# Optimization experiments

Hardware: AMD Instinct MI355X
Metric: run time of the kernel (lower is better)

## Reference

```python
import jax, jax.numpy as jnp
import numpy as np

H, C = 6, 32  # heads, per-head channels (concat=False -> mean over heads)
NEG_SLOPE = 0.2


def gat_layer(x, edge_index, W, a_src, a_dst, b):
    # PyG GATConv (shared lin, add_self_loops=True, concat=False, bias)
    N = x.shape[0]
    xh = (x @ W).reshape(N, H, C)                      # [N,H,C]
    alpha_src = (xh * a_src).sum(-1)                   # [N,H]
    alpha_dst = (xh * a_dst).sum(-1)                   # [N,H]
    loops = jnp.arange(N, dtype=edge_index.dtype)
    src = jnp.concatenate([edge_index[0], loops])
    dst = jnp.concatenate([edge_index[1], loops])
    e = jax.nn.leaky_relu(alpha_src[src] + alpha_dst[dst], NEG_SLOPE)  # [E,H]
    # segment softmax over incoming edges of each destination node
    m = jax.ops.segment_max(e, dst, num_segments=N)
    e = jnp.exp(e - m[dst])
    denom = jax.ops.segment_sum(e, dst, num_segments=N)
    alpha = e / (denom[dst] + 1e-16)                   # [E,H]
    out = jax.ops.segment_sum(alpha[:, :, None] * xh[src], dst, num_segments=N)  # [N,H,C]
    return out.mean(axis=1) + b                        # [N,C]


def setup_inputs() -> dict:
    key = jax.random.key(0)
    ks = jax.random.split(key, 20)
    B, E = 50000, 800000
    NU, NI, D = 100000, 50000, 32
    s = 0.1
    inp = {}
    inp['user'] = jax.random.randint(ks[0], (B,), 0, NU)
    inp['item'] = jax.random.randint(ks[1], (B,), 0, NI)
    inp['graph'] = jax.random.randint(ks[2], (2, E), 0, B)
    inp['u_table'] = jax.random.normal(ks[3], (NU, D), jnp.float32) * s
    inp['i_table'] = jax.random.normal(ks[4], (NI, D), jnp.float32) * s
    # GAT layer 1: in=32 -> heads*32
    inp['W1'] = jax.random.normal(ks[5], (D, H * C), jnp.float32) * s
    inp['a_src1'] = jax.random.normal(ks[6], (H, C), jnp.float32) * s
    inp['a_dst1'] = jax.random.normal(ks[7], (H, C), jnp.float32) * s
    inp['b1'] = jnp.zeros((C,), jnp.float32)
    # GAT layer 2: in=32 -> heads*32
    inp['W2'] = jax.random.normal(ks[8], (C, H * C), jnp.float32) * s
    inp['a_src2'] = jax.random.normal(ks[9], (H, C), jnp.float32) * s
    inp['a_dst2'] = jax.random.normal(ks[10], (H, C), jnp.float32) * s
    inp['b2'] = jnp.zeros((C,), jnp.float32)
    # MLP head: (C + D)=64 -> 64 -> 1
    inp['lw1'] = jax.random.normal(ks[11], (C + D, 64), jnp.float32) * s
    inp['lb1'] = jnp.zeros((64,), jnp.float32)
    inp['lw2'] = jax.random.normal(ks[12], (64, 1), jnp.float32) * s
    inp['lb2'] = jnp.zeros((1,), jnp.float32)
    return inp


def reference(user, item, graph, u_table, i_table, W1, a_src1, a_dst1, b1,
              W2, a_src2, a_dst2, b2, lw1, lb1, lw2, lb2):
    u_emb = u_table[user]                              # [B, 32]
    i_emb = i_table[item]                              # [B, 32]
    i_emb = gat_layer(i_emb, graph, W1, a_src1, a_dst1, b1)
    i_emb = gat_layer(i_emb, graph, W2, a_src2, a_dst2, b2)
    out = jnp.concatenate([u_emb, i_emb], axis=1)      # [B, 64]
    out = out @ lw1 + lb1
    out = out @ lw2 + lb2                              # [B, 1]
    return jax.nn.sigmoid(out)
```

## Files before the change

### kernel.cpp

```cpp
#include <hip/hip_runtime.h>
#include <hip/hip_fp16.h>
#include <math.h>

#define NEG_SLOPE 0.2f
#define TILE 16
#define BKB2 8
#define CHUNK 16384

__global__ void k_init(
    const float* __restrict__ W1, const float* __restrict__ as1,
    const float* __restrict__ ad1,
    const float* __restrict__ W2, const float* __restrict__ as2,
    const float* __restrict__ ad2,
    const float* __restrict__ lw1, const float* __restrict__ lb1,
    const float* __restrict__ lw2, const float* __restrict__ lb2,
    float* __restrict__ wsd1, float* __restrict__ wsd2,
    float* __restrict__ weff,
    unsigned int* __restrict__ whalf1, unsigned int* __restrict__ whalf2,
    int* __restrict__ bcnt, int NBK)
{
    int t = threadIdx.x;
    if (t <= NBK) bcnt[t] = 0;
    if (t < 768) {
        int layer = (t >= 384);
        int r = t - layer * 384;
        int k = r / 12, j = r - k * 12;
        const float* W = layer ? W2 : W1;
        const float* a = (j < 6) ? (layer ? as2 : as1) : (layer ? ad2 : ad1);
        int h = (j < 6) ? j : j - 6;
        float acc = 0.f;
        #pragma unroll
        for (int c = 0; c < 32; ++c)
            acc = fmaf(W[k * 192 + h * 32 + c], a[h * 32 + c], acc);
        (layer ? wsd2 : wsd1)[k * 12 + j] = acc;
    } else {
        int i = t - 768;
        float acc = 0.f;
        for (int o = 0; o < 64; ++o) acc += lw1[i * 64 + o] * lw2[o];
        weff[i] = acc;
        if (i == 0) {
            float b = lb2[0];
            for (int o = 0; o < 64; ++o) b += lb1[o] * lw2[o];
            weff[64] = b;
        }
    }
    if (t < 384) {
        int layer = (t >= 192);
        int col = t - layer * 192;
        const float* W = layer ? W2 : W1;
        unsigned int* dst = layer ? whalf2 : whalf1;
        #pragma unroll
        for (int i = 0; i < 16; ++i) {
            __half2 p = __floats2half2_rn(W[(2 * i) * 192 + col],
                                          W[(2 * i + 1) * 192 + col]);
            dst[col * 16 + i] = *(unsigned int*)&p;
        }
    }
}

__global__ __launch_bounds__(256) void k_hist_prep(
    const int* __restrict__ g, int E, int* __restrict__ bcnt,
    int* __restrict__ blockbase, int NBK, int NBLK,
    const float* __restrict__ xf, const int* __restrict__ gidx,
    const float* __restrict__ wsd, __half* __restrict__ xp,
    float* __restrict__ asrc, float* __restrict__ adst, int N)
{
    __shared__ int hist[256];
    __shared__ float xs[TILE * 33];
    __shared__ int   rows[TILE];
    __shared__ float wsd_s[384];
    const int t = threadIdx.x;
    if (blockIdx.x < NBLK) {
        const int blk = blockIdx.x;
        hist[t] = 0;
        __syncthreads();
        const int base = blk * CHUNK;
        const int end = min(base + CHUNK, E);
        for (int e = base + t; e < end; e += 256)
            atomicAdd(&hist[g[E + e] >> BKB2], 1);
        __syncthreads();
        if (t < NBK) {
            int c = hist[t];
            blockbase[blk * NBK + t] = c ? atomicAdd(&bcnt[t], c) : 0;
        }
    } else {
        const int n0 = (blockIdx.x - NBLK) * TILE;
        for (int i = t; i < 384; i += 256) wsd_s[i] = wsd[i];
        if (t < TILE) {
            int n = n0 + t;
            rows[t] = (n < N) ? gidx[n] : -1;
        }
        __syncthreads();
        if (t < TILE * 8) {
            int m = t >> 3, q = t & 7;
            int r = rows[m];
            float4 v = (r >= 0) ? *(const float4*)(xf + (size_t)r * 32 + q * 4)
                                : make_float4(0.f, 0.f, 0.f, 0.f);
            float* dst = xs + m * 33 + q * 4;
            dst[0] = v.x; dst[1] = v.y; dst[2] = v.z; dst[3] = v.w;
            if (r >= 0) {
                __half2 p0 = __floats2half2_rn(v.x, v.y);
                __half2 p1 = __floats2half2_rn(v.z, v.w);
                uint2 u; u.x = *(unsigned int*)&p0; u.y = *(unsigned int*)&p1;
                *(uint2*)((unsigned int*)xp + (size_t)(n0 + m) * 16 + q * 2) = u;
            }
        }
        __syncthreads();
        if (t < 192) {
            const int m = t / 12, j = t - m * 12;
            const int n = n0 + m;
            if (n < N) {
                const float* xr = xs + m * 33;
                float a = 0.f;
                #pragma unroll
                for (int k = 0; k < 32; ++k)
                    a = fmaf(xr[k], wsd_s[k * 12 + j], a);
                if (j < 6) asrc[(size_t)n * 8 + j] = a;
                else       adst[(size_t)n * 8 + (j - 6)] = a;
            }
        }
    }
}

__device__ __forceinline__ int scan_excl_256(int v, int* wsum)
{
    const int t = threadIdx.x, lane = t & 63, w = t >> 6;
    int incl = v;
    #pragma unroll
    for (int off = 1; off < 64; off <<= 1) {
        int u = __shfl_up(incl, off);
        if (lane >= off) incl += u;
    }
    if (lane == 63) wsum[w] = incl;
    __syncthreads();
    int base = 0;
    for (int q = 0; q < w; ++q) base += wsum[q];
    return base + incl - v;
}

__global__ __launch_bounds__(256) void k_bin2(
    const int* __restrict__ g, int E, const int* __restrict__ bcnt,
    const int* __restrict__ blockbase, int* __restrict__ pairs, int NBK)
{
    __shared__ int cur[256];
    __shared__ int wsum[4];
    const int t = threadIdx.x, blk = blockIdx.x;
    const int v = (t < NBK) ? bcnt[t] : 0;
    const int excl = scan_excl_256(v, wsum);
    if (t < NBK) cur[t] = excl + blockbase[blk * NBK + t];
    __syncthreads();
    const int base = blk * CHUNK;
    const int end = min(base + CHUNK, E);
    for (int e = base + t; e < end; e += 256) {
        int s = g[e], d = g[E + e];
        int pos = atomicAdd(&cur[d >> BKB2], 1);
        pairs[pos] = (s << 8) | (d & 255);
    }
}

__global__ __launch_bounds__(256) void k_build(
    const int* __restrict__ pairs, const int* __restrict__ bcnt,
    int* __restrict__ rowptr, int* __restrict__ deg, int* __restrict__ adj,
    int N, int NBK)
{
    __shared__ int cnt[256];
    __shared__ int cur[256];
    __shared__ int wsum[4];
    __shared__ int lohi[2];
    const int b = blockIdx.x, t = threadIdx.x;
    {
        const int v = (t < NBK) ? bcnt[t] : 0;
        const int excl = scan_excl_256(v, wsum);
        if (t == b) { lohi[0] = excl; lohi[1] = excl + v; }
    }
    cnt[t] = 0;
    __syncthreads();
    const int lo = lohi[0], hi = lohi[1];
    for (int i = lo + t; i < hi; i += 256)
        atomicAdd(&cnt[pairs[i] & 255], 1);
    __syncthreads();
    const int v = cnt[t];
    __syncthreads();
    const int excl = scan_excl_256(v, wsum);
    const int node = b * 256 + t;
    const int abase = lo + b * 256;
    if (node < N) {
        const int rp = abase + excl + t;
        rowptr[node] = rp;
        deg[node] = v + 1;
        adj[rp] = node;
        cur[t] = rp + 1;
    } else cur[t] = 0;
    __syncthreads();
    for (int i = lo + t; i < hi; i += 256) {
        int p = pairs[i];
        int pos = atomicAdd(&cur[p & 255], 1);
        adj[pos] = p >> 8;
    }
}

__global__ __launch_bounds__(256) void k_gat(
    const int* __restrict__ rowptr, const int* __restrict__ deg,
    const int* __restrict__ adj,
    const float* __restrict__ asrc, const float* __restrict__ adst,
    const __half* __restrict__ xp, __half* __restrict__ zn, int N)
{
    __shared__ float4 st[4][32];
    const int wv = threadIdx.x >> 6;
    const int n = blockIdx.x * 4 + wv;
    if (n >= N) return;
    const int lane = threadIdx.x & 63;
    const int half = lane >> 5;
    const int c = lane & 31;
    const int el = lane & 31;

    const float* adr = adst + (size_t)n * 8;
    const float ad0 = adr[0], ad1 = adr[1], ad2 = adr[2];
    const float ad3 = adr[3], ad4 = adr[4], ad5 = adr[5];

    const int start = rowptr[n];
    const int dg = deg[n];
    const char* xcb = (const char*)xp + c * 2;

    __half2 acc0 = __float2half2_rn(0.f);
    __half2 acc1 = __float2half2_rn(0.f);
    __half2 acc2 = __float2half2_rn(0.f);
    float dl0 = 0.f, dl1 = 0.f, dl2 = 0.f, dl3 = 0.f, dl4 = 0.f, dl5 = 0.f;

    for (int base = 0; base < dg; base += 32) {
        const int rem = dg - base;
        const bool valid = el < rem;
        const int s = valid ? adj[start + base + el] : 0;
        const float4* a4 = (const float4*)(asrc + (size_t)s * 8);
        const float4 A = a4[0], Bv = a4[1];
        float v0 = A.x + ad0, v1 = A.y + ad1, v2 = A.z + ad2;
        float v3 = A.w + ad3, v4 = Bv.x + ad4, v5 = Bv.y + ad5;
        v0 = fmaxf(v0, NEG_SLOPE * v0); v1 = fmaxf(v1, NEG_SLOPE * v1);
        v2 = fmaxf(v2, NEG_SLOPE * v2); v3 = fmaxf(v3, NEG_SLOPE * v3);
        v4 = fmaxf(v4, NEG_SLOPE * v4); v5 = fmaxf(v5, NEG_SLOPE * v5);
        const float w0 = valid ? __expf(v0) : 0.f;
        const float w1 = valid ? __expf(v1) : 0.f;
        const float w2 = valid ? __expf(v2) : 0.f;
        const float w3 = valid ? __expf(v3) : 0.f;
        const float w4 = valid ? __expf(v4) : 0.f;
        const float w5 = valid ? __expf(v5) : 0.f;
        dl0 += w0; dl1 += w1; dl2 += w2; dl3 += w3; dl4 += w4; dl5 += w5;
        float4 rec;
        rec.x = __int_as_float(s * 64);
        const __half2 w01 = __floats2half2_rn(w0, w1);
        const __half2 w23 = __floats2half2_rn(w2, w3);
        const __half2 w45 = __floats2half2_rn(w4, w5);
        rec.y = *(const float*)&w01;
        rec.z = *(const float*)&w23;
        rec.w = *(const float*)&w45;
        if (lane < 32) st[wv][el] = rec;

        const int cnt = min(32, rem);
        const int nh = (((cnt + 1) >> 1) + 3) & ~3;
        for (int i = 0; i < nh; i += 4) {
            #pragma unroll
            for (int q = 0; q < 4; ++q) {
                const float4 r = st[wv][2 * (i + q) + half];
                const __half xval = *(const __half*)(xcb + __float_as_int(r.x));
                const __half2 xv2 = __half2half2(xval);
                acc0 = __hfma2(*(const __half2*)&r.y, xv2, acc0);
                acc1 = __hfma2(*(const __half2*)&r.z, xv2, acc1);
                acc2 = __hfma2(*(const __half2*)&r.w, xv2, acc2);
            }
        }
    }
    {
        int b0 = __shfl_xor(*(const int*)&acc0, 32);
        int b1 = __shfl_xor(*(const int*)&acc1, 32);
        int b2 = __shfl_xor(*(const int*)&acc2, 32);
        acc0 = __hadd2(acc0, *(const __half2*)&b0);
        acc1 = __hadd2(acc1, *(const __half2*)&b1);
        acc2 = __hadd2(acc2, *(const __half2*)&b2);
    }
    #pragma unroll
    for (int o = 1; o <= 16; o <<= 1) {
        dl0 += __shfl_xor(dl0, o); dl1 += __shfl_xor(dl1, o);
        dl2 += __shfl_xor(dl2, o); dl3 += __shfl_xor(dl3, o);
        dl4 += __shfl_xor(dl4, o); dl5 += __shfl_xor(dl5, o);
    }
    if (half == 0) {
        __half* zr = zn + (size_t)n * 192 + c;
        zr[0]   = __float2half(__low2float(acc0)  / dl0);
        zr[32]  = __float2half(__high2float(acc0) / dl1);
        zr[64]  = __float2half(__low2float(acc1)  / dl2);
        zr[96]  = __float2half(__high2float(acc1) / dl3);
        zr[128] = __float2half(__low2float(acc2)  / dl4);
        zr[160] = __float2half(__high2float(acc2) / dl5);
    }
}

template<int FUSE>
__global__ __launch_bounds__(192) void k_post(
    const __half* __restrict__ zn, const unsigned int* __restrict__ whalf,
    const float* __restrict__ bias, __half* __restrict__ yout,
    const float* __restrict__ wsd,
    float* __restrict__ asrc, float* __restrict__ adst,
    const int* __restrict__ user, const float* __restrict__ u_table,
    const float* __restrict__ weff, float* __restrict__ outp, int N)
{
    __shared__ unsigned int znl[TILE][96];
    __shared__ float part[TILE][192];
    __shared__ float ys[TILE][33];
    __shared__ float wsd_s[384];
    const int t = threadIdx.x;
    const int h = t >> 5, c = t & 31;
    const int n0 = blockIdx.x * TILE;

    const uint4* wq = (const uint4*)(whalf + (size_t)t * 16);
    const uint4 w0 = wq[0], w1 = wq[1], w2 = wq[2], w3 = wq[3];
    if (FUSE == 0)
        for (int i = t; i < 384; i += 192) wsd_s[i] = wsd[i];

    {
        const int m = t / 12, slot = t - m * 12;
        const int n = n0 + m;
        if (n < N) {
            const uint4* src = (const uint4*)((const unsigned int*)zn
                               + (size_t)n * 96 + slot * 8);
            uint4 a = src[0], b = src[1];
            uint4* d = (uint4*)&znl[m][slot * 8];
            d[0] = a; d[1] = b;
        }
    }
    __syncthreads();

    #define DOT4(W) { \
        unsigned int zz0 = zp[0], zz1 = zp[1], zz2 = zp[2], zz3 = zp[3]; \
        acc2 = __hfma2(*(__half2*)&zz0, *(__half2*)&W.x, acc2); \
        acc2 = __hfma2(*(__half2*)&zz1, *(__half2*)&W.y, acc2); \
        acc2 = __hfma2(*(__half2*)&zz2, *(__half2*)&W.z, acc2); \
        acc2 = __hfma2(*(__half2*)&zz3, *(__half2*)&W.w, acc2); zp += 4; }

    #pragma unroll 4
    for (int m = 0; m < TILE; ++m) {
        const unsigned int* zp = &znl[m][h * 16];
        __half2 acc2 = __float2half2_rn(0.f);
        DOT4(w0) DOT4(w1) DOT4(w2) DOT4(w3)
        part[m][t] = __low2float(acc2) + __high2float(acc2);
    }
    #undef DOT4
    __syncthreads();

    #pragma unroll
    for (int mb = 0; mb < 3; ++mb) {
        const int m = mb * 6 + h;
        const int n = n0 + m;
        if (m < TILE && n < N) {
            const float y = (part[m][c] + part[m][32 + c] + part[m][64 + c]
                           + part[m][96 + c] + part[m][128 + c]
                           + part[m][160 + c]) * (1.f / 6.f) + bias[c];
            if (FUSE == 0) {
                yout[(size_t)n * 32 + c] = __float2half(y);
                ys[m][c] = y;
            } else {
                const float u = u_table[(size_t)user[n] * 32 + c];
                float p = fmaf(y, weff[32 + c], u * weff[c]);
                #pragma unroll
                for (int o = 16; o > 0; o >>= 1) p += __shfl_xor(p, o);
                if (c == 0) outp[n] = 1.f / (1.f + __expf(-(p + weff[64])));
            }
        }
    }
    if (FUSE == 0) {
        __syncthreads();
        const int m = t / 12, j = t - m * 12;
        const int n = n0 + m;
        if (n < N) {
            const float* yr = ys[m];
            float a = 0.f;
            #pragma unroll
            for (int k = 0; k < 32; ++k) a = fmaf(yr[k], wsd_s[k * 12 + j], a);
            if (j < 6) asrc[(size_t)n * 8 + j] = a;
            else       adst[(size_t)n * 8 + (j - 6)] = a;
        }
    }
}


extern "C" void kernel_launch(void* const* d_in, const int* in_sizes, int n_in,
                              void* d_out, int out_size, void* d_ws, size_t ws_size,
                              hipStream_t stream)
{
    const int*   user    = (const int*)  d_in[0];
    const int*   item    = (const int*)  d_in[1];
    const int*   graph   = (const int*)  d_in[2];
    const float* u_table = (const float*)d_in[3];
    const float* i_table = (const float*)d_in[4];
    const float* W1      = (const float*)d_in[5];
    const float* a_src1  = (const float*)d_in[6];
    const float* a_dst1  = (const float*)d_in[7];
    const float* b1      = (const float*)d_in[8];
    const float* W2      = (const float*)d_in[9];
    const float* a_src2  = (const float*)d_in[10];
    const float* a_dst2  = (const float*)d_in[11];
    const float* b2      = (const float*)d_in[12];
    const float* lw1     = (const float*)d_in[13];
    const float* lb1     = (const float*)d_in[14];
    const float* lw2     = (const float*)d_in[15];
    const float* lb2     = (const float*)d_in[16];

    const int B  = in_sizes[0];
    const int N  = B;
    const int E  = in_sizes[2] / 2;
    const int Et = E + N;
    const int NBK = (N + 255) / 256;
    const int NBLK = (E + CHUNK - 1) / CHUNK;

    float* ws = (float*)d_ws;
    size_t off = 0;
    __half* xp1   = (__half*)(ws + off); off += (size_t)N * 16;
    __half* y1h   = (__half*)(ws + off); off += (size_t)N * 16;
    __half* zn    = (__half*)(ws + off); off += (size_t)N * 96;
    float* asrc   = ws + off; off += (size_t)N * 8;
    float* adst   = ws + off; off += (size_t)N * 8;
    float* wsd1   = ws + off; off += 384;
    float* wsd2   = ws + off; off += 384;
    float* weff   = ws + off; off += 128;
    unsigned int* whalf1 = (unsigned int*)(ws + off); off += 3072;
    unsigned int* whalf2 = (unsigned int*)(ws + off); off += 3072;
    int*   deg    = (int*)(ws + off); off += N;
    int*   rowptr = (int*)(ws + off); off += N;
    int*   bcnt   = (int*)(ws + off); off += NBK + 1;
    int*   bbase  = (int*)(ws + off); off += (size_t)NBLK * NBK;
    int*   adj    = (int*)(ws + off); off += Et + 2;
    int*   pairs  = (int*)(ws + off); off += E;

    const int ggrid = (N + 3) / 4;
    const int pgrid = (N + TILE - 1) / TILE;

    hipLaunchKernelGGL(k_init, dim3(1), dim3(832), 0, stream,
        W1, a_src1, a_dst1, W2, a_src2, a_dst2,
        lw1, lb1, lw2, lb2, wsd1, wsd2, weff, whalf1, whalf2, bcnt, NBK);
    hipLaunchKernelGGL(k_hist_prep, dim3(NBLK + pgrid), dim3(256), 0, stream,
        graph, E, bcnt, bbase, NBK, NBLK,
        i_table, item, wsd1, xp1, asrc, adst, N);
    hipLaunchKernelGGL(k_bin2, dim3(NBLK), dim3(256), 0, stream,
        graph, E, bcnt, bbase, pairs, NBK);
    hipLaunchKernelGGL(k_build, dim3(NBK), dim3(256), 0, stream,
        pairs, bcnt, rowptr, deg, adj, N, NBK);
    hipLaunchKernelGGL(k_gat, dim3(ggrid), dim3(256), 0, stream,
        rowptr, deg, adj, asrc, adst, xp1, zn, N);
    hipLaunchKernelGGL(k_post<0>, dim3(pgrid), dim3(192), 0, stream,
        zn, whalf1, b1, y1h, wsd2, asrc, adst,
        (const int*)nullptr, (const float*)nullptr,
        (const float*)nullptr, (float*)nullptr, N);
    hipLaunchKernelGGL(k_gat, dim3(ggrid), dim3(256), 0, stream,
        rowptr, deg, adj, asrc, adst, y1h, zn, N);
    hipLaunchKernelGGL(k_post<1>, dim3(pgrid), dim3(192), 0, stream,
        zn, whalf2, b2, (__half*)nullptr, (const float*)nullptr,
        (float*)nullptr, (float*)nullptr,
        user, u_table, weff, (float*)d_out, N);
}
```

Before: 170.9 us.

## Process two destination nodes per wavefront, one per half-wave, in GAT aggregation

The GAT aggregation kernel now assigns two destination nodes to each 64-lane wavefront, with each 32-lane half handling one node's edges and channels. Before, both halves shared one node and split its edges, then needed a cross-half shuffle reduction. The change is meant to use all lanes for edge-weight computation, drop that reduction and halve the number of waves. In exchange, each half loops to the larger of the two nodes' degrees, so degree imbalance adds wasted iterations.

After: 154.7 us. -9.5%, faster.

```diff
diff --git a/kernel.cpp b/kernel.cpp
--- a/kernel.cpp
+++ b/kernel.cpp
@@ -205,21 +205,22 @@
     const float* __restrict__ asrc, const float* __restrict__ adst,
     const __half* __restrict__ xp, __half* __restrict__ zn, int N)
 {
-    __shared__ float4 st[4][32];
+    __shared__ float4 st[4][2][32];
     const int wv = threadIdx.x >> 6;
-    const int n = blockIdx.x * 4 + wv;
-    if (n >= N) return;
     const int lane = threadIdx.x & 63;
     const int half = lane >> 5;
     const int c = lane & 31;
-    const int el = lane & 31;
-
-    const float* adr = adst + (size_t)n * 8;
+    const int n = blockIdx.x * 8 + wv * 2 + half;
+    const bool nvalid = (n < N);
+    const int nsafe = nvalid ? n : 0;
+
+    const float* adr = adst + (size_t)nsafe * 8;
     const float ad0 = adr[0], ad1 = adr[1], ad2 = adr[2];
     const float ad3 = adr[3], ad4 = adr[4], ad5 = adr[5];
 
-    const int start = rowptr[n];
-    const int dg = deg[n];
+    const int start = rowptr[nsafe];
+    const int dg = nvalid ? deg[nsafe] : 1;
+    const int dgmax = max(dg, __shfl_xor(dg, 32));
     const char* xcb = (const char*)xp + c * 2;
 
     __half2 acc0 = __float2half2_rn(0.f);
@@ -227,10 +228,10 @@
     __half2 acc2 = __float2half2_rn(0.f);
     float dl0 = 0.f, dl1 = 0.f, dl2 = 0.f, dl3 = 0.f, dl4 = 0.f, dl5 = 0.f;
 
-    for (int base = 0; base < dg; base += 32) {
+    for (int base = 0; base < dgmax; base += 32) {
         const int rem = dg - base;
-        const bool valid = el < rem;
-        const int s = valid ? adj[start + base + el] : 0;
+        const bool valid = nvalid && (c < rem);
+        const int s = valid ? adj[start + base + c] : 0;
         const float4* a4 = (const float4*)(asrc + (size_t)s * 8);
         const float4 A = a4[0], Bv = a4[1];
         float v0 = A.x + ad0, v1 = A.y + ad1, v2 = A.z + ad2;
@@ -253,14 +254,14 @@
         rec.y = *(const float*)&w01;
         rec.z = *(const float*)&w23;
         rec.w = *(const float*)&w45;
-        if (lane < 32) st[wv][el] = rec;
-
-        const int cnt = min(32, rem);
-        const int nh = (((cnt + 1) >> 1) + 3) & ~3;
+        st[wv][half][c] = rec;
+
+        const int cntw = min(32, dgmax - base);
+        const int nh = (cntw + 3) & ~3;
         for (int i = 0; i < nh; i += 4) {
             #pragma unroll
             for (int q = 0; q < 4; ++q) {
-                const float4 r = st[wv][2 * (i + q) + half];
+                const float4 r = st[wv][half][i + q];
                 const __half xval = *(const __half*)(xcb + __float_as_int(r.x));
                 const __half2 xv2 = __half2half2(xval);
                 acc0 = __hfma2(*(const __half2*)&r.y, xv2, acc0);
@@ -269,21 +270,13 @@
             }
         }
     }
-    {
-        int b0 = __shfl_xor(*(const int*)&acc0, 32);
-        int b1 = __shfl_xor(*(const int*)&acc1, 32);
-        int b2 = __shfl_xor(*(const int*)&acc2, 32);
-        acc0 = __hadd2(acc0, *(const __half2*)&b0);
-        acc1 = __hadd2(acc1, *(const __half2*)&b1);
-        acc2 = __hadd2(acc2, *(const __half2*)&b2);
-    }
     #pragma unroll
     for (int o = 1; o <= 16; o <<= 1) {
         dl0 += __shfl_xor(dl0, o); dl1 += __shfl_xor(dl1, o);
         dl2 += __shfl_xor(dl2, o); dl3 += __shfl_xor(dl3, o);
         dl4 += __shfl_xor(dl4, o); dl5 += __shfl_xor(dl5, o);
     }
-    if (half == 0) {
+    if (nvalid) {
         __half* zr = zn + (size_t)n * 192 + c;
         zr[0]   = __float2half(__low2float(acc0)  / dl0);
         zr[32]  = __float2half(__high2float(acc0) / dl1);
@@ -430,7 +423,7 @@
     int*   adj    = (int*)(ws + off); off += Et + 2;
     int*   pairs  = (int*)(ws + off); off += E;
 
-    const int ggrid = (N + 3) / 4;
+    const int ggrid = (N + 7) / 8;
     const int pgrid = (N + TILE - 1) / TILE;
 
     hipLaunchKernelGGL(k_init, dim3(1), dim3(832), 0, stream,
```
